# Kernel optimization log

Hardware: AMD Instinct MI355X
Metric: run time of the kernel (lower is better)

## Reference

```python
import jax, jax.numpy as jnp
import numpy as np


def setup_inputs() -> dict:
    key = jax.random.key(0)
    ks = jax.random.split(key, 8)
    B, H, W, C = 4, 64, 64, 64
    d = C // 8
    x = jax.random.normal(ks[0], (B, H, W, C), dtype=jnp.float32)
    # 1x1 conv kernels (spectral-normalized in the original; here we use the
    # already-normalized weight matrices directly, scaled to unit-ish norm)
    Wf = jax.random.normal(ks[1], (C, d), dtype=jnp.float32) * (1.0 / np.sqrt(C))
    bf = jnp.zeros((d,), dtype=jnp.float32)
    Wg = jax.random.normal(ks[2], (C, d), dtype=jnp.float32) * (1.0 / np.sqrt(C))
    bg = jnp.zeros((d,), dtype=jnp.float32)
    Wh = jax.random.normal(ks[3], (C, C), dtype=jnp.float32) * (1.0 / np.sqrt(C))
    bh = jnp.zeros((C,), dtype=jnp.float32)
    gamma = jnp.float32(1.0)
    return {"x": x, "Wf": Wf, "bf": bf, "Wg": Wg, "bg": bg,
            "Wh": Wh, "bh": bh, "gamma": gamma}


def reference(x, Wf, bf, Wg, bg, Wh, bh, gamma):
    # x: [B, H, W, C] (NHWC, as Keras Conv2D default)
    B, H, W, C = x.shape
    N = H * W
    # 1x1 convs == per-pixel channel matmuls
    q = jnp.einsum('bhwc,cd->bhwd', x, Wf) + bf   # [B,H,W,C//8]
    k = jnp.einsum('bhwc,cd->bhwd', x, Wg) + bg   # [B,H,W,C//8]
    v = jnp.einsum('bhwc,cd->bhwd', x, Wh) + bh   # [B,H,W,C]
    q = q.reshape(B, N, -1)
    k = k.reshape(B, N, -1)
    v = v.reshape(B, N, C)
    # full non-causal attention (no 1/sqrt(d) scaling in the original)
    s = jnp.einsum('bnd,bmd->bnm', q, k)          # [B,N,N]
    s = jax.nn.softmax(s, axis=-1)
    o = jnp.einsum('bnm,bmc->bnc', s, v)          # [B,N,C]
    o = o.reshape(B, H, W, C)
    return gamma * o + x
```

## Files before the change

### kernel.cpp

```cpp
#include <hip/hip_runtime.h>
#include <hip/hip_bf16.h>

#define BATCH 4
#define NTOK 4096
#define CCH 64
#define KSPLIT 4
#define KPB (NTOK / KSPLIT)
#define NTILE (KPB / 64)
#define TPW (NTILE / 4)

#define QSCALE 184.66496523f
#define SBIAS  16251.0f

typedef short s16x8 __attribute__((ext_vector_type(8)));
typedef float f32x4 __attribute__((ext_vector_type(4)));

static __device__ __forceinline__ unsigned short f2bf(float f) {
    union { __hip_bfloat16 h; unsigned short u; } cv;
    cv.h = __float2bfloat16(f);
    return cv.u;
}
static __device__ __forceinline__ float bf2f(unsigned short u) {
    union { unsigned int u; float f; } c; c.u = ((unsigned)u) << 16;
    return c.f;
}
static __device__ __forceinline__ float bf_split(float f, unsigned short& h) {
    h = f2bf(f);
    return f - bf2f(h);
}
static __device__ __forceinline__ unsigned pack_rne(float a, float b) {
    return ((unsigned)f2bf(b) << 16) | f2bf(a);
}
static __device__ __forceinline__ unsigned pack_bits(float a, float b) {
    return ((unsigned)(int)b << 16) | (unsigned)(int)a;
}

__global__ __launch_bounds__(256) void proj_kernel(
    const float* __restrict__ xg,
    const float* __restrict__ Wf, const float* __restrict__ bf_,
    const float* __restrict__ Wg, const float* __restrict__ bg,
    const float* __restrict__ Wh, const float* __restrict__ bh,
    unsigned short* __restrict__ Qp, unsigned short* __restrict__ Kp,
    unsigned short* __restrict__ vTg)
{
    __shared__ float xS[32 * 68];
    __shared__ unsigned short xbS[32 * 72];
    __shared__ float WfT[8 * 68];
    __shared__ float WgT[8 * 68];
    __shared__ unsigned short vtS[64 * 40];

    const int t = threadIdx.x;
    const int b = blockIdx.x >> 7;
    const int n0 = (blockIdx.x & 127) * 32;

    const float* xrow = xg + ((size_t)b * NTOK + n0) * CCH;
    for (int f = t; f < 512; f += 256) {
        int r = f >> 4, c4 = (f & 15) * 4;
        float4 v = *(const float4*)(xrow + r * 64 + c4);
        *(float4*)(xS + r * 68 + c4) = v;
        uint2 pk = { pack_rne(v.x, v.y), pack_rne(v.z, v.w) };
        *(uint2*)(xbS + r * 72 + c4) = pk;
    }
    for (int e = t; e < 512; e += 256) {
        int ci = e >> 3, j = e & 7;
        WfT[j * 68 + ci] = Wf[e];
        WgT[j * 68 + ci] = Wg[e];
    }
    __syncthreads();

    const int w = t >> 6, lane = t & 63, ml = lane & 15, quad = lane >> 4;

    {
        s16x8 a0, a1;
        #pragma unroll
        for (int j = 0; j < 8; ++j) {
            a0[j] = (short)f2bf(Wh[(quad * 8 + j) * 64 + w * 16 + ml]);
            a1[j] = (short)f2bf(Wh[(32 + quad * 8 + j) * 64 + w * 16 + ml]);
        }
        #pragma unroll
        for (int nf = 0; nf < 2; ++nf) {
            int tok = nf * 16 + ml;
            s16x8 b0 = *(const s16x8*)(xbS + tok * 72 + quad * 8);
            s16x8 b1 = *(const s16x8*)(xbS + tok * 72 + 32 + quad * 8);
            f32x4 cc = __builtin_amdgcn_mfma_f32_16x16x32_bf16(a0, b0, (f32x4){0.f,0.f,0.f,0.f}, 0, 0, 0);
            cc = __builtin_amdgcn_mfma_f32_16x16x32_bf16(a1, b1, cc, 0, 0, 0);
            #pragma unroll
            for (int reg = 0; reg < 4; ++reg) {
                int cout = w * 16 + quad * 4 + reg;
                vtS[cout * 40 + nf * 16 + ml] = f2bf(cc[reg] + bh[cout]);
            }
        }
    }

    {
        int r = t >> 3, j = t & 7;
        float q = bf_[j], k = bg[j];
        for (int ci = 0; ci < 64; ci += 4) {
            float4 x4 = *(const float4*)(xS + r * 68 + ci);
            float4 wf4 = *(const float4*)(WfT + j * 68 + ci);
            float4 wg4 = *(const float4*)(WgT + j * 68 + ci);
            q += x4.x * wf4.x + x4.y * wf4.y + x4.z * wf4.z + x4.w * wf4.w;
            k += x4.x * wg4.x + x4.y * wg4.y + x4.z * wg4.z + x4.w * wg4.w;
        }
        q *= QSCALE;
        unsigned short qh, kh;
        float qres = bf_split(q, qh);
        float kres = bf_split(k, kh);
        unsigned short ql = f2bf(qres), kl = f2bf(kres);
        size_t qbase = ((size_t)b * NTOK + n0 + r) * 32;
        Qp[qbase + j]      = qh;
        Qp[qbase + 8 + j]  = ql;
        Qp[qbase + 16 + j] = qh;
        Qp[qbase + 24 + j] = 0;
        size_t kbase = ((size_t)b * NTOK + n0 + r) * 16;
        Kp[kbase + j]     = kh;
        Kp[kbase + 8 + j] = kl;
    }
    __syncthreads();

    {
        int c_ = t >> 2, chunk = t & 3;
        uint4 v = *(const uint4*)(vtS + c_ * 40 + chunk * 8);
        *(uint4*)(vTg + ((size_t)b * CCH + c_) * NTOK + n0 + chunk * 8) = v;
    }
}

__global__ __launch_bounds__(256, 3) void attn_kernel(
    const unsigned short* __restrict__ Qp,
    const unsigned short* __restrict__ Kp,
    const unsigned short* __restrict__ vTg,
    unsigned short* __restrict__ Opart,
    float* __restrict__ lpart)
{
    __shared__ unsigned short KC[KPB * 16];

    const int t = threadIdx.x;
    const int blk = blockIdx.x;
    const int b = blk >> 8;
    const int qt = (blk >> 2) & 63;
    const int ks = blk & 3;
    const int m0 = qt * 64;
    const int kb0 = ks * KPB;
    const int w = t >> 6, lane = t & 63;
    const int ml = lane & 15, quad = lane >> 4;

    const unsigned short* qpb = Qp + (size_t)b * NTOK * 32;
    const unsigned short* kpb = Kp + (size_t)b * NTOK * 16;
    const unsigned short* vtb = vTg + (size_t)b * CCH * NTOK;

    for (int kk = t; kk < KPB; kk += 256) {
        const unsigned short* src = kpb + (size_t)(kb0 + kk) * 16;
        *(uint4*)(&KC[kk * 16])     = *(const uint4*)(src);
        *(uint4*)(&KC[kk * 16 + 8]) = *(const uint4*)(src + 8);
    }

    s16x8 qf[4];
    #pragma unroll
    for (int qg = 0; qg < 4; ++qg)
        qf[qg] = *(const s16x8*)(qpb + (size_t)(m0 + qg * 16 + ml) * 32 + quad * 8);

    const int keyA = 8 * (ml >> 2) + (ml & 3);
    const int khsel = (quad == 2) ? 8 : 0;

    s16x8 ones;
    #pragma unroll
    for (int i = 0; i < 8; ++i) ones[i] = (short)0x3F80;

    f32x4 o[4][4];
    f32x4 lac[4];
    #pragma unroll
    for (int cg = 0; cg < 4; ++cg)
        #pragma unroll
        for (int qg = 0; qg < 4; ++qg) o[cg][qg] = (f32x4){0.f,0.f,0.f,0.f};
    #pragma unroll
    for (int qg = 0; qg < 4; ++qg) lac[qg] = (f32x4){0.f,0.f,0.f,0.f};
    const f32x4 sb = {SBIAS, SBIAS, SBIAS, SBIAS};

    __syncthreads();

    const int tile0 = w * TPW;
    s16x8 kf0 = *(const s16x8*)(&KC[(tile0 * 64 + keyA) * 16 + khsel]);
    s16x8 kf1 = *(const s16x8*)(&KC[(tile0 * 64 + keyA + 4) * 16 + khsel]);
    s16x8 kf2 = *(const s16x8*)(&KC[(tile0 * 64 + 32 + keyA) * 16 + khsel]);
    s16x8 kf3 = *(const s16x8*)(&KC[(tile0 * 64 + 36 + keyA) * 16 + khsel]);

    for (int i = 0; i < TPW; ++i) {
        const int tile = w * TPW + i;
        const int kb = kb0 + tile * 64;

        s16x8 vf[4][2];
        #pragma unroll
        for (int cg = 0; cg < 4; ++cg) {
            const unsigned short* vr = vtb + (size_t)(cg * 16 + ml) * NTOK + kb + quad * 8;
            vf[cg][0] = *(const s16x8*)(vr);
            vf[cg][1] = *(const s16x8*)(vr + 32);
        }
        const int tn = (i + 1 < TPW) ? tile + 1 : tile0;
        s16x8 kn0 = *(const s16x8*)(&KC[(tn * 64 + keyA) * 16 + khsel]);
        s16x8 kn1 = *(const s16x8*)(&KC[(tn * 64 + keyA + 4) * 16 + khsel]);
        s16x8 kn2 = *(const s16x8*)(&KC[(tn * 64 + 32 + keyA) * 16 + khsel]);
        s16x8 kn3 = *(const s16x8*)(&KC[(tn * 64 + 36 + keyA) * 16 + khsel]);

        union { unsigned u[4]; s16x8 h; } P0[4], P1[4];
        #pragma unroll
        for (int qg = 0; qg < 4; ++qg) {
            f32x4 sA0 = __builtin_amdgcn_mfma_f32_16x16x32_bf16(kf0, qf[qg], sb, 0, 0, 0);
            f32x4 sB0 = __builtin_amdgcn_mfma_f32_16x16x32_bf16(kf1, qf[qg], sb, 0, 0, 0);
            f32x4 sA1 = __builtin_amdgcn_mfma_f32_16x16x32_bf16(kf2, qf[qg], sb, 0, 0, 0);
            f32x4 sB1 = __builtin_amdgcn_mfma_f32_16x16x32_bf16(kf3, qf[qg], sb, 0, 0, 0);
            P0[qg].u[0] = pack_bits(sA0[0], sA0[1]);
            P0[qg].u[1] = pack_bits(sA0[2], sA0[3]);
            P0[qg].u[2] = pack_bits(sB0[0], sB0[1]);
            P0[qg].u[3] = pack_bits(sB0[2], sB0[3]);
            P1[qg].u[0] = pack_bits(sA1[0], sA1[1]);
            P1[qg].u[1] = pack_bits(sA1[2], sA1[3]);
            P1[qg].u[2] = pack_bits(sB1[0], sB1[1]);
            P1[qg].u[3] = pack_bits(sB1[2], sB1[3]);
        }
        kf0 = kn0; kf1 = kn1; kf2 = kn2; kf3 = kn3;

        #pragma unroll
        for (int qg = 0; qg < 4; ++qg) {
            lac[qg] = __builtin_amdgcn_mfma_f32_16x16x32_bf16(ones, P0[qg].h, lac[qg], 0, 0, 0);
            lac[qg] = __builtin_amdgcn_mfma_f32_16x16x32_bf16(ones, P1[qg].h, lac[qg], 0, 0, 0);
        }
        #pragma unroll
        for (int cg = 0; cg < 4; ++cg)
            #pragma unroll
            for (int qg = 0; qg < 4; ++qg) {
                o[cg][qg] = __builtin_amdgcn_mfma_f32_16x16x32_bf16(vf[cg][0], P0[qg].h, o[cg][qg], 0, 0, 0);
                o[cg][qg] = __builtin_amdgcn_mfma_f32_16x16x32_bf16(vf[cg][1], P1[qg].h, o[cg][qg], 0, 0, 0);
            }
    }

    float* OL = (float*)KC;
    float* lL = OL + 64 * 68;
    #pragma unroll
    for (int r = 0; r < 4; ++r) {
        __syncthreads();
        if (w == r) {
            #pragma unroll
            for (int cg = 0; cg < 4; ++cg)
                #pragma unroll
                for (int qg = 0; qg < 4; ++qg) {
                    f32x4* p = (f32x4*)(&OL[(qg * 16 + ml) * 68 + cg * 16 + quad * 4]);
                    if (r == 0) *p = o[cg][qg];
                    else {
                        f32x4 v = *p;
                        v[0] += o[cg][qg][0]; v[1] += o[cg][qg][1];
                        v[2] += o[cg][qg][2]; v[3] += o[cg][qg][3];
                        *p = v;
                    }
                }
            if (quad == 0) {
                #pragma unroll
                for (int qg = 0; qg < 4; ++qg) {
                    if (r == 0) lL[qg * 16 + ml] = lac[qg][0];
                    else        lL[qg * 16 + ml] += lac[qg][0];
                }
            }
        }
    }
    __syncthreads();

    {
        int q = t >> 2, c0 = (t & 3) * 16;
        alignas(16) unsigned short us[16];
        #pragma unroll
        for (int k = 0; k < 16; ++k) us[k] = f2bf(OL[q * 68 + c0 + k]);
        size_t obase = ((size_t)ks * (BATCH * NTOK) + (size_t)b * NTOK + m0 + q) * 64 + c0;
        *(uint4*)(Opart + obase)     = *(uint4*)(us);
        *(uint4*)(Opart + obase + 8) = *(uint4*)(us + 8);
    }
    if (t < 64)
        lpart[ks * (BATCH * NTOK) + b * NTOK + m0 + t] = lL[t];
}

__global__ __launch_bounds__(256) void combine_kernel(
    const float* __restrict__ xg,
    const unsigned short* __restrict__ Opart,
    const float* __restrict__ lpart,
    const float* __restrict__ gammaPtr,
    float* __restrict__ out)
{
    const int i4 = blockIdx.x * 256 + threadIdx.x;
    const int base = i4 * 4;
    const int tok = base >> 6;

    float lsum = 0.f;
    #pragma unroll
    for (int s = 0; s < KSPLIT; ++s)
        lsum += lpart[s * (BATCH * NTOK) + tok];

    float o0 = 0.f, o1 = 0.f, o2 = 0.f, o3 = 0.f;
    #pragma unroll
    for (int s = 0; s < KSPLIT; ++s) {
        uint2 u = *(const uint2*)(Opart + (size_t)s * (BATCH * NTOK * 64) + base);
        o0 += bf2f((unsigned short)(u.x & 0xFFFF));
        o1 += bf2f((unsigned short)(u.x >> 16));
        o2 += bf2f((unsigned short)(u.y & 0xFFFF));
        o3 += bf2f((unsigned short)(u.y >> 16));
    }
    const float4 x4 = *(const float4*)(xg + base);
    const float gi = gammaPtr[0] / lsum;
    float4 r;
    r.x = gi * o0 + x4.x;
    r.y = gi * o1 + x4.y;
    r.z = gi * o2 + x4.z;
    r.w = gi * o3 + x4.w;
    *(float4*)(out + base) = r;
}

extern "C" void kernel_launch(void* const* d_in, const int* in_sizes, int n_in,
                              void* d_out, int out_size, void* d_ws, size_t ws_size,
                              hipStream_t stream) {
    const float* x  = (const float*)d_in[0];
    const float* Wf = (const float*)d_in[1];
    const float* bf = (const float*)d_in[2];
    const float* Wg = (const float*)d_in[3];
    const float* bg = (const float*)d_in[4];
    const float* Wh = (const float*)d_in[5];
    const float* bh = (const float*)d_in[6];
    const float* gamma = (const float*)d_in[7];
    float* out = (float*)d_out;

    char* ws = (char*)d_ws;
    unsigned short* Qp    = (unsigned short*)ws;
    unsigned short* Kp    = (unsigned short*)(ws + (1u << 20));
    unsigned short* vTg   = (unsigned short*)(ws + (2u << 20));
    unsigned short* Opart = (unsigned short*)(ws + (4u << 20));
    float*          lpart = (float*)(ws + (12u << 20));

    proj_kernel<<<BATCH * 128, 256, 0, stream>>>(x, Wf, bf, Wg, bg, Wh, bh,
                                                 Qp, Kp, vTg);
    attn_kernel<<<BATCH * 64 * KSPLIT, 256, 0, stream>>>(Qp, Kp, vTg, Opart, lpart);
    combine_kernel<<<(BATCH * NTOK * CCH) / 1024, 256, 0, stream>>>(x, Opart, lpart, gamma, out);
}
```

Measured before the change: 113.2 us.

## Drop key split and fuse combine step into attention kernel epilogue

Removes the 4-way split over keys so each block processes all 4096 keys for its 64 queries, and applies the normalization, gamma and residual directly in the attention epilogue. This eliminates the combine kernel launch and the bf16 partial output and sum round-trips through global memory. K fragments are now read from global memory instead of being staged in LDS. The grid shrinks to 256 blocks at one block per CU, which lowers occupancy and parallelism.

Result: faster. 108.4 us (-4.3%).

```diff
diff --git a/kernel.cpp b/kernel.cpp
--- a/kernel.cpp
+++ b/kernel.cpp
@@ -4,10 +4,7 @@
 #define BATCH 4
 #define NTOK 4096
 #define CCH 64
-#define KSPLIT 4
-#define KPB (NTOK / KSPLIT)
-#define NTILE (KPB / 64)
-#define TPW (NTILE / 4)
+#define TPW 16
 
 #define QSCALE 184.66496523f
 #define SBIAS  16251.0f
@@ -125,22 +122,21 @@
     }
 }
 
-__global__ __launch_bounds__(256, 3) void attn_kernel(
+__global__ __launch_bounds__(256, 1) void attn_kernel(
+    const float* __restrict__ xg,
     const unsigned short* __restrict__ Qp,
     const unsigned short* __restrict__ Kp,
     const unsigned short* __restrict__ vTg,
-    unsigned short* __restrict__ Opart,
-    float* __restrict__ lpart)
+    const float* __restrict__ gammaPtr,
+    float* __restrict__ out)
 {
-    __shared__ unsigned short KC[KPB * 16];
+    __shared__ float OL[64 * 68];
+    __shared__ float lL[64];
 
     const int t = threadIdx.x;
-    const int blk = blockIdx.x;
-    const int b = blk >> 8;
-    const int qt = (blk >> 2) & 63;
-    const int ks = blk & 3;
+    const int b = blockIdx.x >> 6;
+    const int qt = blockIdx.x & 63;
     const int m0 = qt * 64;
-    const int kb0 = ks * KPB;
     const int w = t >> 6, lane = t & 63;
     const int ml = lane & 15, quad = lane >> 4;
 
@@ -148,12 +144,6 @@
     const unsigned short* kpb = Kp + (size_t)b * NTOK * 16;
     const unsigned short* vtb = vTg + (size_t)b * CCH * NTOK;
 
-    for (int kk = t; kk < KPB; kk += 256) {
-        const unsigned short* src = kpb + (size_t)(kb0 + kk) * 16;
-        *(uint4*)(&KC[kk * 16])     = *(const uint4*)(src);
-        *(uint4*)(&KC[kk * 16 + 8]) = *(const uint4*)(src + 8);
-    }
-
     s16x8 qf[4];
     #pragma unroll
     for (int qg = 0; qg < 4; ++qg)
@@ -176,17 +166,15 @@
     for (int qg = 0; qg < 4; ++qg) lac[qg] = (f32x4){0.f,0.f,0.f,0.f};
     const f32x4 sb = {SBIAS, SBIAS, SBIAS, SBIAS};
 
-    __syncthreads();
-
     const int tile0 = w * TPW;
-    s16x8 kf0 = *(const s16x8*)(&KC[(tile0 * 64 + keyA) * 16 + khsel]);
-    s16x8 kf1 = *(const s16x8*)(&KC[(tile0 * 64 + keyA + 4) * 16 + khsel]);
-    s16x8 kf2 = *(const s16x8*)(&KC[(tile0 * 64 + 32 + keyA) * 16 + khsel]);
-    s16x8 kf3 = *(const s16x8*)(&KC[(tile0 * 64 + 36 + keyA) * 16 + khsel]);
+    s16x8 kf0 = *(const s16x8*)(kpb + (size_t)(tile0 * 64 + keyA) * 16 + khsel);
+    s16x8 kf1 = *(const s16x8*)(kpb + (size_t)(tile0 * 64 + keyA + 4) * 16 + khsel);
+    s16x8 kf2 = *(const s16x8*)(kpb + (size_t)(tile0 * 64 + 32 + keyA) * 16 + khsel);
+    s16x8 kf3 = *(const s16x8*)(kpb + (size_t)(tile0 * 64 + 36 + keyA) * 16 + khsel);
 
     for (int i = 0; i < TPW; ++i) {
-        const int tile = w * TPW + i;
-        const int kb = kb0 + tile * 64;
+        const int tile = tile0 + i;
+        const int kb = tile * 64;
 
         s16x8 vf[4][2];
         #pragma unroll
@@ -196,10 +184,10 @@
             vf[cg][1] = *(const s16x8*)(vr + 32);
         }
         const int tn = (i + 1 < TPW) ? tile + 1 : tile0;
-        s16x8 kn0 = *(const s16x8*)(&KC[(tn * 64 + keyA) * 16 + khsel]);
-        s16x8 kn1 = *(const s16x8*)(&KC[(tn * 64 + keyA + 4) * 16 + khsel]);
-        s16x8 kn2 = *(const s16x8*)(&KC[(tn * 64 + 32 + keyA) * 16 + khsel]);
-        s16x8 kn3 = *(const s16x8*)(&KC[(tn * 64 + 36 + keyA) * 16 + khsel]);
+        s16x8 kn0 = *(const s16x8*)(kpb + (size_t)(tn * 64 + keyA) * 16 + khsel);
+        s16x8 kn1 = *(const s16x8*)(kpb + (size_t)(tn * 64 + keyA + 4) * 16 + khsel);
+        s16x8 kn2 = *(const s16x8*)(kpb + (size_t)(tn * 64 + 32 + keyA) * 16 + khsel);
+        s16x8 kn3 = *(const s16x8*)(kpb + (size_t)(tn * 64 + 36 + keyA) * 16 + khsel);
 
         union { unsigned u[4]; s16x8 h; } P0[4], P1[4];
         #pragma unroll
@@ -233,8 +221,6 @@
             }
     }
 
-    float* OL = (float*)KC;
-    float* lL = OL + 64 * 68;
     #pragma unroll
     for (int r = 0; r < 4; ++r) {
         __syncthreads();
@@ -264,51 +250,21 @@
     __syncthreads();
 
     {
+        const float gamma = gammaPtr[0];
         int q = t >> 2, c0 = (t & 3) * 16;
-        alignas(16) unsigned short us[16];
-        #pragma unroll
-        for (int k = 0; k < 16; ++k) us[k] = f2bf(OL[q * 68 + c0 + k]);
-        size_t obase = ((size_t)ks * (BATCH * NTOK) + (size_t)b * NTOK + m0 + q) * 64 + c0;
-        *(uint4*)(Opart + obase)     = *(uint4*)(us);
-        *(uint4*)(Opart + obase + 8) = *(uint4*)(us + 8);
-    }
-    if (t < 64)
-        lpart[ks * (BATCH * NTOK) + b * NTOK + m0 + t] = lL[t];
-}
-
-__global__ __launch_bounds__(256) void combine_kernel(
-    const float* __restrict__ xg,
-    const unsigned short* __restrict__ Opart,
-    const float* __restrict__ lpart,
-    const float* __restrict__ gammaPtr,
-    float* __restrict__ out)
-{
-    const int i4 = blockIdx.x * 256 + threadIdx.x;
-    const int base = i4 * 4;
-    const int tok = base >> 6;
-
-    float lsum = 0.f;
-    #pragma unroll
-    for (int s = 0; s < KSPLIT; ++s)
-        lsum += lpart[s * (BATCH * NTOK) + tok];
-
-    float o0 = 0.f, o1 = 0.f, o2 = 0.f, o3 = 0.f;
-    #pragma unroll
-    for (int s = 0; s < KSPLIT; ++s) {
-        uint2 u = *(const uint2*)(Opart + (size_t)s * (BATCH * NTOK * 64) + base);
-        o0 += bf2f((unsigned short)(u.x & 0xFFFF));
-        o1 += bf2f((unsigned short)(u.x >> 16));
-        o2 += bf2f((unsigned short)(u.y & 0xFFFF));
-        o3 += bf2f((unsigned short)(u.y >> 16));
-    }
-    const float4 x4 = *(const float4*)(xg + base);
-    const float gi = gammaPtr[0] / lsum;
-    float4 r;
-    r.x = gi * o0 + x4.x;
-    r.y = gi * o1 + x4.y;
-    r.z = gi * o2 + x4.z;
-    r.w = gi * o3 + x4.w;
-    *(float4*)(out + base) = r;
+        const float gi = gamma / lL[q];
+        size_t base = ((size_t)b * NTOK + m0 + q) * CCH + c0;
+        #pragma unroll
+        for (int c4 = 0; c4 < 16; c4 += 4) {
+            float4 x4 = *(const float4*)(xg + base + c4);
+            float4 r;
+            r.x = gi * OL[q * 68 + c0 + c4 + 0] + x4.x;
+            r.y = gi * OL[q * 68 + c0 + c4 + 1] + x4.y;
+            r.z = gi * OL[q * 68 + c0 + c4 + 2] + x4.z;
+            r.w = gi * OL[q * 68 + c0 + c4 + 3] + x4.w;
+            *(float4*)(out + base + c4) = r;
+        }
+    }
 }
 
 extern "C" void kernel_launch(void* const* d_in, const int* in_sizes, int n_in,
@@ -325,14 +281,11 @@
     float* out = (float*)d_out;
 
     char* ws = (char*)d_ws;
-    unsigned short* Qp    = (unsigned short*)ws;
-    unsigned short* Kp    = (unsigned short*)(ws + (1u << 20));
-    unsigned short* vTg   = (unsigned short*)(ws + (2u << 20));
-    unsigned short* Opart = (unsigned short*)(ws + (4u << 20));
-    float*          lpart = (float*)(ws + (12u << 20));
+    unsigned short* Qp  = (unsigned short*)ws;
+    unsigned short* Kp  = (unsigned short*)(ws + (1u << 20));
+    unsigned short* vTg = (unsigned short*)(ws + (2u << 20));
 
     proj_kernel<<<BATCH * 128, 256, 0, stream>>>(x, Wf, bf, Wg, bg, Wh, bh,
                                                  Qp, Kp, vTg);
-    attn_kernel<<<BATCH * 64 * KSPLIT, 256, 0, stream>>>(Qp, Kp, vTg, Opart, lpart);
-    combine_kernel<<<(BATCH * NTOK * CCH) / 1024, 256, 0, stream>>>(x, Opart, lpart, gamma, out);
-}
+    attn_kernel<<<BATCH * 64, 256, 0, stream>>>(x, Qp, Kp, vTg, gamma, out);
+}
```
